# Optimization experiments

Measured on AMD Instinct MI355X. Metric: run time of the kernel, lower is better.

## Reference

```python
import jax, jax.numpy as jnp
import numpy as np

B, T, F, U, OUT_STEPS = 128, 256, 64, 1024, 32
D_HID = 32  # dense head hidden width


def lstm_step(h, c, x, W, R, b):
    # Keras gate order: i, f, g (cell candidate), o
    z = x @ W + h @ R + b  # [B, 4U]
    i, f, g, o = jnp.split(z, 4, axis=-1)
    c_new = jax.nn.sigmoid(f) * c + jax.nn.sigmoid(i) * jnp.tanh(g)
    h_new = jax.nn.sigmoid(o) * jnp.tanh(c_new)
    return h_new, c_new


def setup_inputs() -> dict:
    key = jax.random.key(0)
    ks = jax.random.split(key, 16)
    s = 0.05  # small init scale to keep gates unsaturated
    return {
        "inputs": jax.random.normal(ks[0], (B, T, F), jnp.float32),
        # encoder LSTM layer (input dim F)
        "Wl": jax.random.normal(ks[1], (F, 4 * U), jnp.float32) * s,
        "Rl": jax.random.normal(ks[2], (U, 4 * U), jnp.float32) * s,
        "bl": jnp.zeros((4 * U,), jnp.float32),
        "Wc": jax.random.normal(ks[3], (F, 4 * U), jnp.float32) * s,
        "Rc": jax.random.normal(ks[4], (U, 4 * U), jnp.float32) * s,
        "bc": jnp.zeros((4 * U,), jnp.float32),
        # rnn_cell (an LSTMCell; input dim = units, fed lstm_cell output)
        "Wr": jax.random.normal(ks[5], (U, 4 * U), jnp.float32) * s,
        "Rr": jax.random.normal(ks[6], (U, 4 * U), jnp.float32) * s,
        "br": jnp.zeros((4 * U,), jnp.float32),
        # dense head: Dense(32, relu) -> Dense(num_features)
        "W1": jax.random.normal(ks[7], (U, D_HID), jnp.float32) * s,
        "b1": jnp.zeros((D_HID,), jnp.float32),
        "W2": jax.random.normal(ks[8], (D_HID, F), jnp.float32) * s,
        "b2": jnp.zeros((F,), jnp.float32),
    }


def reference(inputs, Wl, Rl, bl, Wc, Rc, bc, Wr, Rr, br, W1, b1, W2, b2):
    b = inputs.shape[0]
    h0 = jnp.zeros((b, U), inputs.dtype)
    c0 = jnp.zeros((b, U), inputs.dtype)

    def enc_step(carry, x_t):
        h, c = carry
        h, c = lstm_step(h, c, x_t, Wl, Rl, bl)
        return (h, c), None

    # encoder LSTM over time (scan over T, batch-parallel)
    (h, c), _ = jax.lax.scan(enc_step, (h0, c0), jnp.swapaxes(inputs, 0, 1))

    dense = lambda x: jax.nn.relu(x @ W1 + b1) @ W2 + b2

    pred0 = dense(h)  # [B, F]
    # state_rnn initialized from encoder final state (same values, evolves separately)
    init = (pred0, h, c, h, c)

    def ar_step(carry, _):
        pred, hl, cl, hr, cr = carry
        hl, cl = lstm_step(hl, cl, pred, Wc, Rc, bc)
        hr, cr = lstm_step(hr, cr, hl, Wr, Rr, br)
        pred = dense(hr)
        return (pred, hl, cl, hr, cr), pred

    _, preds = jax.lax.scan(ar_step, init, None, length=OUT_STEPS - 1)
    preds = jnp.concatenate([pred0[None], preds], axis=0)  # [OUT, B, F]
    return jnp.transpose(preds, (1, 0, 2))  # [B, OUT, F]
```

## Files before the change

### kernel.cpp

```cpp
#include <hip/hip_runtime.h>

typedef unsigned short u16;
typedef unsigned int u32;
typedef unsigned long long u64;
typedef short v8s __attribute__((ext_vector_type(8)));
typedef int v4i __attribute__((ext_vector_type(4)));
typedef float f32x4 __attribute__((ext_vector_type(4)));

#define NB 128
#define NU 1024
#define NF 64
#define NT 256
#define NOUT 32
#define NBLK 256
#define XS 72
#define FPAD 32
#define ZBS 66

__device__ __forceinline__ u16 f2bf(float f) {
  union { float f; u32 u; } v; v.f = f;
  u32 x = v.u;
  return (u16)((x + 0x7fffu + ((x >> 16) & 1u)) >> 16);
}
__device__ __forceinline__ float bf2f(u16 u) {
  union { u32 u; float f; } v; v.u = ((u32)u) << 16;
  return v.f;
}

__device__ __forceinline__ void cstore32(u32* p, u32 v) {
  __hip_atomic_store(p, v, __ATOMIC_RELAXED, __HIP_MEMORY_SCOPE_AGENT);
}
__device__ __forceinline__ v4i cload128(const void* p) {
  v4i r;
  asm volatile("global_load_dwordx4 %0, %1, off sc0 sc1" : "=v"(r) : "v"(p) : "memory");
  return r;
}

__device__ __forceinline__ void publish(u32* bar, u32 gen, int bid, int tid) {
  asm volatile("s_waitcnt vmcnt(0)" ::: "memory");
  __syncthreads();
  if (tid == 0)
    __hip_atomic_store(&bar[bid * FPAD], gen, __ATOMIC_RELAXED, __HIP_MEMORY_SCOPE_AGENT);
}

__device__ __forceinline__ void pollslice(const u32* bar, u32 gen, int grp,
                                          int w, int lane) {
  const u32* fl = bar + (size_t)(grp * 64 + w * 16 + (lane & 15)) * FPAD;
  bool ok = (lane >= 16);
  u32 spin = 0;
  for (;;) {
    if (!ok)
      ok = __hip_atomic_load(fl, __ATOMIC_RELAXED, __HIP_MEMORY_SCOPE_AGENT) >= gen;
    if (__all(ok)) break;
    __builtin_amdgcn_s_sleep(1);
    if (++spin > 4000000u) break;
  }
}

__global__ void init_bar(u32* bar) {
  int i = blockIdx.x * 256 + threadIdx.x;
  if (i < 2 * NBLK * FPAD) bar[i] = 0;
}

__global__ void pack_weights(const float* __restrict__ top, const float* __restrict__ R,
                             int ktop, int nchunk, u16* __restrict__ dst) {
  int line = blockIdx.x * 256 + threadIdx.x;
  int l = line & 63;
  int rest = line >> 6;
  int s = rest & 1; rest >>= 1;
  int kk = rest % nchunk;
  int t  = rest / nchunk;
  if (t >= 256) return;
  int kbase = kk * 64 + s * 32 + (l >> 4) * 8;
  int col = ((l >> 2) & 3) * 1024 + t * 4 + (l & 3);
  v8s o;
#pragma unroll
  for (int j = 0; j < 8; ++j) {
    int k = kbase + j;
    float v = (k < ktop) ? top[(size_t)k * 4096 + col]
                         : R[(size_t)(k - ktop) * 4096 + col];
    o[j] = (short)f2bf(v);
  }
  *(v8s*)(void*)(dst + (size_t)line * 8) = o;
}

__global__ void pack_w1(const float* __restrict__ W1, u16* __restrict__ dst) {
  int id = blockIdx.x * 256 + threadIdx.x;
  int lane = id & 63;
  int line = id >> 6;
  int res = line >> 6;
  int cl = line & 63;
  int c = cl >> 1, nt = cl & 1;
  int krow = c * 32 + ((lane >> 4) * 8);
  int col = nt * 16 + (lane & 15);
  v8s o;
#pragma unroll
  for (int j = 0; j < 8; ++j) {
    float v = W1[(size_t)(krow + j) * 32 + col];
    u16 hi = f2bf(v);
    o[j] = (short)(res ? f2bf(v - bf2f(hi)) : hi);
  }
  *(v8s*)(void*)(dst + (size_t)id * 8) = o;
}

struct P {
  const float* x;
  const u16 *packE, *packC, *packR, *W1f;
  const float *bl, *bc, *br, *b1, *W2, *b2;
  u16 *hxE0, *hxE1, *hxL0, *hxL1, *hxR0, *hxR1;
  float* out;
  u32* bar;
};

__device__ __forceinline__ v8s ldA(const u16* Asb, int row, int unit) {
  return *(const v8s*)(const void*)(Asb + row * 2048 + ((unit ^ (row & 7)) * 8));
}

__device__ __forceinline__ void stage_bar1(u16* Asb, const u32* bar, u32 gen,
                                           int grp, int w, int lane,
                                           const u16* hx, int dstu) {
  pollslice(bar, gen, grp, w, lane);
  v4i t[16];
#pragma unroll
  for (int j = 0; j < 16; ++j) {
    int q = (w * 16 + j) * 64 + lane;
    t[j] = cload128(hx + (size_t)q * 8);
  }
  asm volatile("s_waitcnt vmcnt(0)" ::: "memory");
#pragma unroll
  for (int j = 0; j < 16; ++j) {
    int q = (w * 16 + j) * 64 + lane;
    int sb = q >> 6, rem = q & 63;
    int r = rem >> 1, c8 = rem & 1;
    int u = (dstu + sb * 2 + c8) ^ (r & 7);
    *(v4i*)(void*)(Asb + r * 2048 + u * 8) = t[j];
  }
  __syncthreads();
}

__device__ __forceinline__ void stage_bar2(u16* Asb, const u32* bar, u32 gen,
                                           int grp, int w, int lane,
                                           const u16* hxa, const u16* hxb) {
  pollslice(bar, gen, grp, w, lane);
  v4i a[16], b[16];
#pragma unroll
  for (int j = 0; j < 16; ++j) {
    int q = (w * 16 + j) * 64 + lane;
    a[j] = cload128(hxa + (size_t)q * 8);
  }
#pragma unroll
  for (int j = 0; j < 16; ++j) {
    int q = (w * 16 + j) * 64 + lane;
    b[j] = cload128(hxb + (size_t)q * 8);
  }
  asm volatile("s_waitcnt vmcnt(0)" ::: "memory");
#pragma unroll
  for (int j = 0; j < 16; ++j) {
    int q = (w * 16 + j) * 64 + lane;
    int sb = q >> 6, rem = q & 63;
    int r = rem >> 1, c8 = rem & 1;
    int u = (sb * 2 + c8) ^ (r & 7);
    *(v4i*)(void*)(Asb + r * 2048 + u * 8) = a[j];
  }
#pragma unroll
  for (int j = 0; j < 16; ++j) {
    int q = (w * 16 + j) * 64 + lane;
    int sb = q >> 6, rem = q & 63;
    int r = rem >> 1, c8 = rem & 1;
    int u = (128 + sb * 2 + c8) ^ (r & 7);
    *(v4i*)(void*)(Asb + r * 2048 + u * 8) = b[j];
  }
  __syncthreads();
}

__device__ __forceinline__ void stageX(u16* Xsb, int tid, int m0,
                                       const float* x, int t) {
#pragma unroll
  for (int i = 0; i < 4; ++i) {
    int idx = tid + i * 256;
    int ml = idx >> 5, dw = idx & 31;
    const float* sp = x + ((size_t)(m0 + ml) * NT + t) * NF + dw * 2;
    u32 v = (u32)f2bf(sp[0]) | ((u32)f2bf(sp[1]) << 16);
    *(u32*)(void*)(Xsb + ml * XS + dw * 2) = v;
  }
}

template <int NCH, int XCH>
__device__ __forceinline__ void mfmaSK(f32x4 (&acc)[4][2], const u16* Asb,
                                       const u16* Xsb, const u16* pack,
                                       int linesz, int tile0,
                                       int w, int lane, int quad, int l15) {
  const u16* tb0 = pack + (size_t)(tile0 + 0) * linesz;
  const u16* tb1 = pack + (size_t)(tile0 + 1) * linesz;
  const u16* tb2 = pack + (size_t)(tile0 + 2) * linesz;
  const u16* tb3 = pack + (size_t)(tile0 + 3) * linesz;
  for (int j = w; j < NCH; j += 4) {
    v8s a0, a1;
    if (XCH > 0 && j < XCH) {
      a0 = *(const v8s*)(const void*)(Xsb + l15 * XS + j * 32 + quad * 8);
      a1 = *(const v8s*)(const void*)(Xsb + (16 + l15) * XS + j * 32 + quad * 8);
    } else {
      int u = (j - XCH) * 4 + quad;
      a0 = ldA(Asb, l15, u);
      a1 = ldA(Asb, 16 + l15, u);
    }
    size_t bo = (size_t)(j * 64 + lane) * 8;
    v8s b0 = *(const v8s*)(const void*)(tb0 + bo);
    v8s b1 = *(const v8s*)(const void*)(tb1 + bo);
    v8s b2 = *(const v8s*)(const void*)(tb2 + bo);
    v8s b3 = *(const v8s*)(const void*)(tb3 + bo);
    acc[0][0] = __builtin_amdgcn_mfma_f32_16x16x32_bf16(a0, b0, acc[0][0], 0, 0, 0);
    acc[1][0] = __builtin_amdgcn_mfma_f32_16x16x32_bf16(a0, b1, acc[1][0], 0, 0, 0);
    acc[2][0] = __builtin_amdgcn_mfma_f32_16x16x32_bf16(a0, b2, acc[2][0], 0, 0, 0);
    acc[3][0] = __builtin_amdgcn_mfma_f32_16x16x32_bf16(a0, b3, acc[3][0], 0, 0, 0);
    acc[0][1] = __builtin_amdgcn_mfma_f32_16x16x32_bf16(a1, b0, acc[0][1], 0, 0, 0);
    acc[1][1] = __builtin_amdgcn_mfma_f32_16x16x32_bf16(a1, b1, acc[1][1], 0, 0, 0);
    acc[2][1] = __builtin_amdgcn_mfma_f32_16x16x32_bf16(a1, b2, acc[2][1], 0, 0, 0);
    acc[3][1] = __builtin_amdgcn_mfma_f32_16x16x32_bf16(a1, b3, acc[3][1], 0, 0, 0);
  }
}

__device__ __forceinline__ void gates_store(float* zb, u16* hpk,
                                            int w, int lane, int quad, int l15,
                                            int wgn, int bid,
                                            const f32x4 (&acc)[4][2],
                                            const float* bias,
                                            float cpair[2], u16* hxout, bool czero) {
  __syncthreads();
#pragma unroll
  for (int tt = 0; tt < 4; ++tt)
#pragma unroll
    for (int rt = 0; rt < 2; ++rt)
#pragma unroll
      for (int r = 0; r < 4; ++r)
        zb[(size_t)(w * 32 + rt * 16 + quad * 4 + r) * ZBS + tt * 16 + l15] =
            acc[tt][rt][r];
  __syncthreads();
  const int tblk = wgn * 4 + w;
#pragma unroll
  for (int rep = 0; rep < 2; ++rep) {
    int pp = lane + rep * 64;
    int ml = pp >> 2;
    int cc = pp & 3;
    int col = tblk * 4 + cc;
    float zg[4];
#pragma unroll
    for (int g = 0; g < 4; ++g) {
      int zc = w * 16 + g * 4 + cc;
      float s = zb[(size_t)(0 * 32 + ml) * ZBS + zc] +
                zb[(size_t)(1 * 32 + ml) * ZBS + zc] +
                zb[(size_t)(2 * 32 + ml) * ZBS + zc] +
                zb[(size_t)(3 * 32 + ml) * ZBS + zc];
      zg[g] = s + bias[g * 1024 + col];
    }
    float cold = czero ? 0.f : cpair[rep];
    float si = 1.f / (1.f + __expf(-zg[0]));
    float sf = 1.f / (1.f + __expf(-zg[1]));
    float so = 1.f / (1.f + __expf(-zg[3]));
    float e2g = __expf(2.f * zg[2]);
    float tg  = (e2g - 1.f) / (e2g + 1.f);
    float cn  = sf * cold + si * tg;
    float e2c = __expf(2.f * cn);
    float tc  = (e2c - 1.f) / (e2c + 1.f);
    cpair[rep] = cn;
    hpk[w * 128 + ml * 4 + cc] = f2bf(so * tc);
  }
  __syncthreads();
  {
    int tid = w * 64 + lane;
    int r = tid >> 3, c2 = tid & 7;
    int wsrc = c2 >> 1;
    u32 v = *(const u32*)(const void*)(hpk + wsrc * 128 + r * 4 + (c2 & 1) * 2);
    cstore32((u32*)(void*)(hxout + (size_t)bid * 512) + r * 8 + c2, v);
  }
}

__device__ __forceinline__ void dense_head(const P& p, const u16* Asb, float* d1s,
                                           u16* Xsb, int tid, int w, int lane,
                                           int quad, int l15, int m0, int step,
                                           bool wout) {
  const int rt = w >> 1, ct = w & 1;
  const int arow = rt * 16 + l15;
  const u16* wf = p.W1f;
  f32x4 acc0 = {0.f, 0.f, 0.f, 0.f}, acc1 = acc0;
#pragma unroll
  for (int k = 0; k < 16; ++k) {
    v8s b0 = *(const v8s*)(const void*)(wf + ((size_t)((2 * k) * 2 + ct) * 64 + lane) * 8);
    v8s a0 = ldA(Asb, arow, 128 + (2 * k) * 4 + quad);
    v8s b1 = *(const v8s*)(const void*)(wf + ((size_t)((2 * k + 1) * 2 + ct) * 64 + lane) * 8);
    v8s a1 = ldA(Asb, arow, 128 + (2 * k + 1) * 4 + quad);
    acc0 = __builtin_amdgcn_mfma_f32_16x16x32_bf16(a0, b0, acc0, 0, 0, 0);
    acc1 = __builtin_amdgcn_mfma_f32_16x16x32_bf16(a1, b1, acc1, 0, 0, 0);
  }
#pragma unroll
  for (int k = 0; k < 16; ++k) {
    v8s b0 = *(const v8s*)(const void*)(wf + ((size_t)(64 + (2 * k) * 2 + ct) * 64 + lane) * 8);
    v8s a0 = ldA(Asb, arow, 128 + (2 * k) * 4 + quad);
    v8s b1 = *(const v8s*)(const void*)(wf + ((size_t)(64 + (2 * k + 1) * 2 + ct) * 64 + lane) * 8);
    v8s a1 = ldA(Asb, arow, 128 + (2 * k + 1) * 4 + quad);
    acc0 = __builtin_amdgcn_mfma_f32_16x16x32_bf16(a0, b0, acc0, 0, 0, 0);
    acc1 = __builtin_amdgcn_mfma_f32_16x16x32_bf16(a1, b1, acc1, 0, 0, 0);
  }
  acc0 += acc1;
  const int col = ct * 16 + l15;
  const float b1c = p.b1[col];
#pragma unroll
  for (int r = 0; r < 4; ++r) {
    int row = rt * 16 + quad * 4 + r;
    d1s[row * 33 + col] = fmaxf(acc0[r] + b1c, 0.f);
  }
  __syncthreads();
  const int r = tid >> 3, cb = (tid & 7) * 8;
  float s2[8];
#pragma unroll
  for (int cc = 0; cc < 8; ++cc) s2[cc] = p.b2[cb + cc];
#pragma unroll
  for (int k = 0; k < 32; ++k) {
    float dv = d1s[r * 33 + k];
    f32x4 w20 = *(const f32x4*)(const void*)(p.W2 + k * 64 + cb);
    f32x4 w21 = *(const f32x4*)(const void*)(p.W2 + k * 64 + cb + 4);
    s2[0] += dv * w20[0]; s2[1] += dv * w20[1];
    s2[2] += dv * w20[2]; s2[3] += dv * w20[3];
    s2[4] += dv * w21[0]; s2[5] += dv * w21[1];
    s2[6] += dv * w21[2]; s2[7] += dv * w21[3];
  }
#pragma unroll
  for (int cc = 0; cc < 8; ++cc) Xsb[r * XS + cb + cc] = f2bf(s2[cc]);
  if (wout) {
    float* po = p.out + ((size_t)(m0 + r) * NOUT + step) * NF + cb;
#pragma unroll
    for (int cc = 0; cc < 8; ++cc) po[cc] = s2[cc];
  }
  __syncthreads();
}

__global__ void __launch_bounds__(256, 1) rnn_persist(P p) {
  __shared__ __align__(16) u16 Asb[32 * 2048];
  __shared__ __align__(16) u16 Xsb[32 * XS];
  __shared__ float d1s[32 * 33];
  __shared__ u16 hpack[512];
  float* zb = (float*)(void*)Asb;

  const int tid = threadIdx.x;
  const int bid = blockIdx.x;
  const int wgn = bid & 63;
  const int mg  = bid >> 6;
  const int m0  = mg * 32;
  const int w    = tid >> 6;
  const int lane = tid & 63;
  const int quad = lane >> 4;
  const int l15  = lane & 15;
  const int tile0 = wgn * 4;
  const size_t gsl = (size_t)mg * 64 * 512;

  float cE2[2] = {0.f, 0.f};
  u32 bno = 0;

  stageX(Xsb, tid, m0, p.x, 0);
  for (int t = 0; t < NT; ++t) {
    const u16* hread = ((t & 1) ? p.hxE1 : p.hxE0) + gsl;
    u16* hwrite      = (t & 1) ? p.hxE0 : p.hxE1;
    f32x4 acc[4][2];
#pragma unroll
    for (int a = 0; a < 4; ++a)
#pragma unroll
      for (int b = 0; b < 2; ++b) acc[a][b] = (f32x4){0.f, 0.f, 0.f, 0.f};
    if (t > 0) {
      stage_bar1(Asb, p.bar, bno, mg, w, lane, hread, 0);
      mfmaSK<34, 2>(acc, Asb, Xsb, p.packE, 17408, tile0, w, lane, quad, l15);
    } else {
      __syncthreads();
      mfmaSK<2, 2>(acc, Asb, Xsb, p.packE, 17408, tile0, w, lane, quad, l15);
    }
    gates_store(zb, hpack, w, lane, quad, l15, wgn, bid, acc,
                p.bl, cE2, hwrite, t == 0);
    if (t + 1 < NT) stageX(Xsb, tid, m0, p.x, t + 1);
    publish(p.bar, ++bno, bid, tid);
  }

  float cL2[2] = {cE2[0], cE2[1]};
  float cR2[2] = {cE2[0], cE2[1]};
  for (int s = 1; s < NOUT; ++s) {
    const u16* hlr = ((s == 1) ? p.hxE0 : ((s & 1) ? p.hxL1 : p.hxL0)) + gsl;
    const u16* hrd = ((s == 1) ? p.hxE0 : ((s & 1) ? p.hxR1 : p.hxR0)) + gsl;
    u16* hlw = (s & 1) ? p.hxL0 : p.hxL1;
    u16* hrw = (s & 1) ? p.hxR0 : p.hxR1;

    {
      stage_bar2(Asb, p.bar, bno, mg, w, lane, hlr, hrd);
      dense_head(p, Asb, d1s, Xsb, tid, w, lane, quad, l15, m0, s - 1, wgn == 0);
      f32x4 acc[4][2];
#pragma unroll
      for (int a = 0; a < 4; ++a)
#pragma unroll
        for (int b = 0; b < 2; ++b) acc[a][b] = (f32x4){0.f, 0.f, 0.f, 0.f};
      mfmaSK<34, 2>(acc, Asb, Xsb, p.packC, 17408, tile0, w, lane, quad, l15);
      gates_store(zb, hpack, w, lane, quad, l15, wgn, bid, acc,
                  p.bc, cL2, hlw, false);
    }
    publish(p.bar, ++bno, bid, tid);

    {
      stage_bar2(Asb, p.bar, bno, mg, w, lane, hlw + gsl, hrd);
      f32x4 acc[4][2];
#pragma unroll
      for (int a = 0; a < 4; ++a)
#pragma unroll
        for (int b = 0; b < 2; ++b) acc[a][b] = (f32x4){0.f, 0.f, 0.f, 0.f};
      mfmaSK<64, 0>(acc, Asb, Xsb, p.packR, 32768, tile0, w, lane, quad, l15);
      gates_store(zb, hpack, w, lane, quad, l15, wgn, bid, acc,
                  p.br, cR2, hrw, false);
    }
    publish(p.bar, ++bno, bid, tid);
  }

  if (wgn == 0) {
    stage_bar1(Asb, p.bar, bno, mg, w, lane, p.hxR0 + gsl, 128);
    dense_head(p, Asb, d1s, Xsb, tid, w, lane, quad, l15, m0, NOUT - 1, true);
  }
}

extern "C" void kernel_launch(void* const* d_in, const int* in_sizes, int n_in,
                              void* d_out, int out_size, void* d_ws, size_t ws_size,
                              hipStream_t stream) {
  const float* x  = (const float*)d_in[0];
  const float* Wl = (const float*)d_in[1];
  const float* Rl = (const float*)d_in[2];
  const float* bl = (const float*)d_in[3];
  const float* Wc = (const float*)d_in[4];
  const float* Rc = (const float*)d_in[5];
  const float* bc = (const float*)d_in[6];
  const float* Wr = (const float*)d_in[7];
  const float* Rr = (const float*)d_in[8];
  const float* br = (const float*)d_in[9];
  const float* W1 = (const float*)d_in[10];
  const float* b1 = (const float*)d_in[11];
  const float* W2 = (const float*)d_in[12];
  const float* b2 = (const float*)d_in[13];

  char* ws = (char*)d_ws;
  size_t off = 0;
  auto alloc = [&](size_t bytes) -> void* {
    void* r = ws + off;
    off += (bytes + 255) & ~(size_t)255;
    return r;
  };
  const size_t szPackE = (size_t)256 * 17408 * 2;
  const size_t szPackR = (size_t)256 * 32768 * 2;
  const size_t szHx    = (size_t)NBLK * 512 * 2;
  u16* packE = (u16*)alloc(szPackE);
  u16* packC = (u16*)alloc(szPackE);
  u16* packR = (u16*)alloc(szPackR);
  u16* W1f   = (u16*)alloc((size_t)128 * 64 * 8 * 2);
  u16* hxE0 = (u16*)alloc(szHx);
  u16* hxE1 = (u16*)alloc(szHx);
  u16* hxL0 = (u16*)alloc(szHx);
  u16* hxL1 = (u16*)alloc(szHx);
  u16* hxR0 = (u16*)alloc(szHx);
  u16* hxR1 = (u16*)alloc(szHx);
  u32* bar = (u32*)alloc(2 * NBLK * FPAD * 4);

  init_bar<<<dim3(64), dim3(256), 0, stream>>>(bar);
  pack_weights<<<dim3(128 * 17), dim3(256), 0, stream>>>(Wl, Rl, 64, 17, packE);
  pack_weights<<<dim3(128 * 17), dim3(256), 0, stream>>>(Wc, Rc, 64, 17, packC);
  pack_weights<<<dim3(128 * 32), dim3(256), 0, stream>>>(Wr, Rr, 1024, 32, packR);
  pack_w1<<<dim3(32), dim3(256), 0, stream>>>(W1, W1f);

  static P p;
  p.x = x;
  p.packE = packE; p.packC = packC; p.packR = packR; p.W1f = W1f;
  p.bl = bl; p.bc = bc; p.br = br;
  p.b1 = b1; p.W2 = W2; p.b2 = b2;
  p.hxE0 = hxE0; p.hxE1 = hxE1;
  p.hxL0 = hxL0; p.hxL1 = hxL1;
  p.hxR0 = hxR0; p.hxR1 = hxR1;
  p.out = (float*)d_out;
  p.bar = bar;

  rnn_persist<<<dim3(NBLK), dim3(256), 0, stream>>>(p);
}
```

Measured before the change: 3.014 ms.

## Split batch across twice as many persistent blocks, 16 rows each

Doubles the persistent grid to 512 blocks, so each block handles 16 batch rows instead of 32. The staging, MFMA accumulators, gate epilogue and dense head are reworked for the smaller tile, and launch bounds now allow two blocks per CU. This aims to spread the serial recurrent work across more CUs and shrink each block's per-step latency. In exchange, every block streams the same weight tiles from L2, so weight traffic doubles, and more blocks must meet at each grid barrier, which adds synchronisation cost.

```diff
diff --git a/kernel.cpp b/kernel.cpp
--- a/kernel.cpp
+++ b/kernel.cpp
@@ -12,7 +12,7 @@
 #define NF 64
 #define NT 256
 #define NOUT 32
-#define NBLK 256
+#define NBLK 512
 #define XS 72
 #define FPAD 32
 #define ZBS 66
@@ -59,7 +59,7 @@
 
 __global__ void init_bar(u32* bar) {
   int i = blockIdx.x * 256 + threadIdx.x;
-  if (i < 2 * NBLK * FPAD) bar[i] = 0;
+  if (i < NBLK * FPAD) bar[i] = 0;
 }
 
 __global__ void pack_weights(const float* __restrict__ top, const float* __restrict__ R,
@@ -120,19 +120,20 @@
                                            int grp, int w, int lane,
                                            const u16* hx, int dstu) {
   pollslice(bar, gen, grp, w, lane);
-  v4i t[16];
-#pragma unroll
-  for (int j = 0; j < 16; ++j) {
-    int q = (w * 16 + j) * 64 + lane;
-    t[j] = cload128(hx + (size_t)q * 8);
+  v4i t[8];
+#pragma unroll
+  for (int j = 0; j < 8; ++j) {
+    int ul = j * 64 + lane;
+    int pl = ul >> 5, q = ul & 31;
+    t[j] = cload128(hx + (size_t)((w * 16 + pl) * 32 + q) * 8);
   }
   asm volatile("s_waitcnt vmcnt(0)" ::: "memory");
 #pragma unroll
-  for (int j = 0; j < 16; ++j) {
-    int q = (w * 16 + j) * 64 + lane;
-    int sb = q >> 6, rem = q & 63;
-    int r = rem >> 1, c8 = rem & 1;
-    int u = (dstu + sb * 2 + c8) ^ (r & 7);
+  for (int j = 0; j < 8; ++j) {
+    int ul = j * 64 + lane;
+    int pl = ul >> 5, q = ul & 31;
+    int r = q >> 1, c8 = q & 1;
+    int u = (dstu + (w * 16 + pl) * 2 + c8) ^ (r & 7);
     *(v4i*)(void*)(Asb + r * 2048 + u * 8) = t[j];
   }
   __syncthreads();
@@ -142,32 +143,34 @@
                                            int grp, int w, int lane,
                                            const u16* hxa, const u16* hxb) {
   pollslice(bar, gen, grp, w, lane);
-  v4i a[16], b[16];
-#pragma unroll
-  for (int j = 0; j < 16; ++j) {
-    int q = (w * 16 + j) * 64 + lane;
-    a[j] = cload128(hxa + (size_t)q * 8);
-  }
-#pragma unroll
-  for (int j = 0; j < 16; ++j) {
-    int q = (w * 16 + j) * 64 + lane;
-    b[j] = cload128(hxb + (size_t)q * 8);
+  v4i a[8], b[8];
+#pragma unroll
+  for (int j = 0; j < 8; ++j) {
+    int ul = j * 64 + lane;
+    int pl = ul >> 5, q = ul & 31;
+    a[j] = cload128(hxa + (size_t)((w * 16 + pl) * 32 + q) * 8);
+  }
+#pragma unroll
+  for (int j = 0; j < 8; ++j) {
+    int ul = j * 64 + lane;
+    int pl = ul >> 5, q = ul & 31;
+    b[j] = cload128(hxb + (size_t)((w * 16 + pl) * 32 + q) * 8);
   }
   asm volatile("s_waitcnt vmcnt(0)" ::: "memory");
 #pragma unroll
-  for (int j = 0; j < 16; ++j) {
-    int q = (w * 16 + j) * 64 + lane;
-    int sb = q >> 6, rem = q & 63;
-    int r = rem >> 1, c8 = rem & 1;
-    int u = (sb * 2 + c8) ^ (r & 7);
+  for (int j = 0; j < 8; ++j) {
+    int ul = j * 64 + lane;
+    int pl = ul >> 5, q = ul & 31;
+    int r = q >> 1, c8 = q & 1;
+    int u = ((w * 16 + pl) * 2 + c8) ^ (r & 7);
     *(v4i*)(void*)(Asb + r * 2048 + u * 8) = a[j];
   }
 #pragma unroll
-  for (int j = 0; j < 16; ++j) {
-    int q = (w * 16 + j) * 64 + lane;
-    int sb = q >> 6, rem = q & 63;
-    int r = rem >> 1, c8 = rem & 1;
-    int u = (128 + sb * 2 + c8) ^ (r & 7);
+  for (int j = 0; j < 8; ++j) {
+    int ul = j * 64 + lane;
+    int pl = ul >> 5, q = ul & 31;
+    int r = q >> 1, c8 = q & 1;
+    int u = (128 + (w * 16 + pl) * 2 + c8) ^ (r & 7);
     *(v4i*)(void*)(Asb + r * 2048 + u * 8) = b[j];
   }
   __syncthreads();
@@ -176,7 +179,7 @@
 __device__ __forceinline__ void stageX(u16* Xsb, int tid, int m0,
                                        const float* x, int t) {
 #pragma unroll
-  for (int i = 0; i < 4; ++i) {
+  for (int i = 0; i < 2; ++i) {
     int idx = tid + i * 256;
     int ml = idx >> 5, dw = idx & 31;
     const float* sp = x + ((size_t)(m0 + ml) * NT + t) * NF + dw * 2;
@@ -186,7 +189,7 @@
 }
 
 template <int NCH, int XCH>
-__device__ __forceinline__ void mfmaSK(f32x4 (&acc)[4][2], const u16* Asb,
+__device__ __forceinline__ void mfmaSK(f32x4 (&acc)[4], const u16* Asb,
                                        const u16* Xsb, const u16* pack,
                                        int linesz, int tile0,
                                        int w, int lane, int quad, int l15) {
@@ -195,65 +198,52 @@
   const u16* tb2 = pack + (size_t)(tile0 + 2) * linesz;
   const u16* tb3 = pack + (size_t)(tile0 + 3) * linesz;
   for (int j = w; j < NCH; j += 4) {
-    v8s a0, a1;
+    v8s a0;
     if (XCH > 0 && j < XCH) {
       a0 = *(const v8s*)(const void*)(Xsb + l15 * XS + j * 32 + quad * 8);
-      a1 = *(const v8s*)(const void*)(Xsb + (16 + l15) * XS + j * 32 + quad * 8);
     } else {
-      int u = (j - XCH) * 4 + quad;
-      a0 = ldA(Asb, l15, u);
-      a1 = ldA(Asb, 16 + l15, u);
+      a0 = ldA(Asb, l15, (j - XCH) * 4 + quad);
     }
     size_t bo = (size_t)(j * 64 + lane) * 8;
     v8s b0 = *(const v8s*)(const void*)(tb0 + bo);
     v8s b1 = *(const v8s*)(const void*)(tb1 + bo);
     v8s b2 = *(const v8s*)(const void*)(tb2 + bo);
     v8s b3 = *(const v8s*)(const void*)(tb3 + bo);
-    acc[0][0] = __builtin_amdgcn_mfma_f32_16x16x32_bf16(a0, b0, acc[0][0], 0, 0, 0);
-    acc[1][0] = __builtin_amdgcn_mfma_f32_16x16x32_bf16(a0, b1, acc[1][0], 0, 0, 0);
-    acc[2][0] = __builtin_amdgcn_mfma_f32_16x16x32_bf16(a0, b2, acc[2][0], 0, 0, 0);
-    acc[3][0] = __builtin_amdgcn_mfma_f32_16x16x32_bf16(a0, b3, acc[3][0], 0, 0, 0);
-    acc[0][1] = __builtin_amdgcn_mfma_f32_16x16x32_bf16(a1, b0, acc[0][1], 0, 0, 0);
-    acc[1][1] = __builtin_amdgcn_mfma_f32_16x16x32_bf16(a1, b1, acc[1][1], 0, 0, 0);
-    acc[2][1] = __builtin_amdgcn_mfma_f32_16x16x32_bf16(a1, b2, acc[2][1], 0, 0, 0);
-    acc[3][1] = __builtin_amdgcn_mfma_f32_16x16x32_bf16(a1, b3, acc[3][1], 0, 0, 0);
+    acc[0] = __builtin_amdgcn_mfma_f32_16x16x32_bf16(a0, b0, acc[0], 0, 0, 0);
+    acc[1] = __builtin_amdgcn_mfma_f32_16x16x32_bf16(a0, b1, acc[1], 0, 0, 0);
+    acc[2] = __builtin_amdgcn_mfma_f32_16x16x32_bf16(a0, b2, acc[2], 0, 0, 0);
+    acc[3] = __builtin_amdgcn_mfma_f32_16x16x32_bf16(a0, b3, acc[3], 0, 0, 0);
   }
 }
 
 __device__ __forceinline__ void gates_store(float* zb, u16* hpk,
                                             int w, int lane, int quad, int l15,
-                                            int wgn, int bid,
-                                            const f32x4 (&acc)[4][2],
+                                            int wgn, int bid, int tid,
+                                            const f32x4 (&acc)[4],
                                             const float* bias,
-                                            float cpair[2], u16* hxout, bool czero) {
+                                            float& creg, u16* hxout, bool czero) {
   __syncthreads();
 #pragma unroll
   for (int tt = 0; tt < 4; ++tt)
 #pragma unroll
-    for (int rt = 0; rt < 2; ++rt)
-#pragma unroll
-      for (int r = 0; r < 4; ++r)
-        zb[(size_t)(w * 32 + rt * 16 + quad * 4 + r) * ZBS + tt * 16 + l15] =
-            acc[tt][rt][r];
-  __syncthreads();
-  const int tblk = wgn * 4 + w;
-#pragma unroll
-  for (int rep = 0; rep < 2; ++rep) {
-    int pp = lane + rep * 64;
-    int ml = pp >> 2;
-    int cc = pp & 3;
-    int col = tblk * 4 + cc;
+    for (int r = 0; r < 4; ++r)
+      zb[(size_t)(w * 16 + quad * 4 + r) * ZBS + tt * 16 + l15] = acc[tt][r];
+  __syncthreads();
+  {
+    int r = tid >> 4, hc = tid & 15;
+    int tt = hc >> 2, cc = hc & 3;
+    int col = wgn * 16 + hc;
     float zg[4];
 #pragma unroll
     for (int g = 0; g < 4; ++g) {
-      int zc = w * 16 + g * 4 + cc;
-      float s = zb[(size_t)(0 * 32 + ml) * ZBS + zc] +
-                zb[(size_t)(1 * 32 + ml) * ZBS + zc] +
-                zb[(size_t)(2 * 32 + ml) * ZBS + zc] +
-                zb[(size_t)(3 * 32 + ml) * ZBS + zc];
+      int zc = tt * 16 + g * 4 + cc;
+      float s = zb[(size_t)(0 * 16 + r) * ZBS + zc] +
+                zb[(size_t)(1 * 16 + r) * ZBS + zc] +
+                zb[(size_t)(2 * 16 + r) * ZBS + zc] +
+                zb[(size_t)(3 * 16 + r) * ZBS + zc];
       zg[g] = s + bias[g * 1024 + col];
     }
-    float cold = czero ? 0.f : cpair[rep];
+    float cold = czero ? 0.f : creg;
     float si = 1.f / (1.f + __expf(-zg[0]));
     float sf = 1.f / (1.f + __expf(-zg[1]));
     float so = 1.f / (1.f + __expf(-zg[3]));
@@ -262,16 +252,14 @@
     float cn  = sf * cold + si * tg;
     float e2c = __expf(2.f * cn);
     float tc  = (e2c - 1.f) / (e2c + 1.f);
-    cpair[rep] = cn;
-    hpk[w * 128 + ml * 4 + cc] = f2bf(so * tc);
-  }
-  __syncthreads();
-  {
-    int tid = w * 64 + lane;
-    int r = tid >> 3, c2 = tid & 7;
-    int wsrc = c2 >> 1;
-    u32 v = *(const u32*)(const void*)(hpk + wsrc * 128 + r * 4 + (c2 & 1) * 2);
-    cstore32((u32*)(void*)(hxout + (size_t)bid * 512) + r * 8 + c2, v);
+    creg = cn;
+    hpk[r * 16 + hc] = f2bf(so * tc);
+  }
+  __syncthreads();
+  if (tid < 128) {
+    int rr = tid >> 3, c2 = tid & 7;
+    u32 v = *(const u32*)(const void*)(hpk + rr * 16 + c2 * 2);
+    cstore32((u32*)(void*)(hxout + (size_t)bid * 256) + rr * 8 + c2, v);
   }
 }
 
@@ -279,107 +267,90 @@
                                            u16* Xsb, int tid, int w, int lane,
                                            int quad, int l15, int m0, int step,
                                            bool wout) {
-  const int rt = w >> 1, ct = w & 1;
-  const int arow = rt * 16 + l15;
+  const int nt = w & 1, kp = w >> 1;
   const u16* wf = p.W1f;
-  f32x4 acc0 = {0.f, 0.f, 0.f, 0.f}, acc1 = acc0;
+  f32x4 aH = {0.f, 0.f, 0.f, 0.f}, aL = aH;
 #pragma unroll
   for (int k = 0; k < 16; ++k) {
-    v8s b0 = *(const v8s*)(const void*)(wf + ((size_t)((2 * k) * 2 + ct) * 64 + lane) * 8);
-    v8s a0 = ldA(Asb, arow, 128 + (2 * k) * 4 + quad);
-    v8s b1 = *(const v8s*)(const void*)(wf + ((size_t)((2 * k + 1) * 2 + ct) * 64 + lane) * 8);
-    v8s a1 = ldA(Asb, arow, 128 + (2 * k + 1) * 4 + quad);
-    acc0 = __builtin_amdgcn_mfma_f32_16x16x32_bf16(a0, b0, acc0, 0, 0, 0);
-    acc1 = __builtin_amdgcn_mfma_f32_16x16x32_bf16(a1, b1, acc1, 0, 0, 0);
-  }
-#pragma unroll
-  for (int k = 0; k < 16; ++k) {
-    v8s b0 = *(const v8s*)(const void*)(wf + ((size_t)(64 + (2 * k) * 2 + ct) * 64 + lane) * 8);
-    v8s a0 = ldA(Asb, arow, 128 + (2 * k) * 4 + quad);
-    v8s b1 = *(const v8s*)(const void*)(wf + ((size_t)(64 + (2 * k + 1) * 2 + ct) * 64 + lane) * 8);
-    v8s a1 = ldA(Asb, arow, 128 + (2 * k + 1) * 4 + quad);
-    acc0 = __builtin_amdgcn_mfma_f32_16x16x32_bf16(a0, b0, acc0, 0, 0, 0);
-    acc1 = __builtin_amdgcn_mfma_f32_16x16x32_bf16(a1, b1, acc1, 0, 0, 0);
-  }
-  acc0 += acc1;
-  const int col = ct * 16 + l15;
-  const float b1c = p.b1[col];
-#pragma unroll
-  for (int r = 0; r < 4; ++r) {
-    int row = rt * 16 + quad * 4 + r;
-    d1s[row * 33 + col] = fmaxf(acc0[r] + b1c, 0.f);
-  }
-  __syncthreads();
-  const int r = tid >> 3, cb = (tid & 7) * 8;
-  float s2[8];
-#pragma unroll
-  for (int cc = 0; cc < 8; ++cc) s2[cc] = p.b2[cb + cc];
-#pragma unroll
-  for (int k = 0; k < 32; ++k) {
-    float dv = d1s[r * 33 + k];
-    f32x4 w20 = *(const f32x4*)(const void*)(p.W2 + k * 64 + cb);
-    f32x4 w21 = *(const f32x4*)(const void*)(p.W2 + k * 64 + cb + 4);
-    s2[0] += dv * w20[0]; s2[1] += dv * w20[1];
-    s2[2] += dv * w20[2]; s2[3] += dv * w20[3];
-    s2[4] += dv * w21[0]; s2[5] += dv * w21[1];
-    s2[6] += dv * w21[2]; s2[7] += dv * w21[3];
-  }
-#pragma unroll
-  for (int cc = 0; cc < 8; ++cc) Xsb[r * XS + cb + cc] = f2bf(s2[cc]);
-  if (wout) {
-    float* po = p.out + ((size_t)(m0 + r) * NOUT + step) * NF + cb;
-#pragma unroll
-    for (int cc = 0; cc < 8; ++cc) po[cc] = s2[cc];
-  }
-  __syncthreads();
-}
-
-__global__ void __launch_bounds__(256, 1) rnn_persist(P p) {
-  __shared__ __align__(16) u16 Asb[32 * 2048];
-  __shared__ __align__(16) u16 Xsb[32 * XS];
-  __shared__ float d1s[32 * 33];
-  __shared__ u16 hpack[512];
+    int c = kp + 2 * k;
+    v8s a  = ldA(Asb, l15, 128 + c * 4 + quad);
+    v8s bh = *(const v8s*)(const void*)(wf + ((size_t)(c * 2 + nt) * 64 + lane) * 8);
+    v8s bl = *(const v8s*)(const void*)(wf + ((size_t)(64 + c * 2 + nt) * 64 + lane) * 8);
+    aH = __builtin_amdgcn_mfma_f32_16x16x32_bf16(a, bh, aH, 0, 0, 0);
+    aL = __builtin_amdgcn_mfma_f32_16x16x32_bf16(a, bl, aL, 0, 0, 0);
+  }
+  aH += aL;
+#pragma unroll
+  for (int r = 0; r < 4; ++r)
+    d1s[kp * 528 + (quad * 4 + r) * 33 + nt * 16 + l15] = aH[r];
+  __syncthreads();
+  {
+    int r = tid >> 4, cb = (tid & 15) * 4;
+    float s2[4];
+#pragma unroll
+    for (int j = 0; j < 4; ++j) s2[j] = p.b2[cb + j];
+#pragma unroll
+    for (int k = 0; k < 32; ++k) {
+      float dv = fmaxf(d1s[r * 33 + k] + d1s[528 + r * 33 + k] + p.b1[k], 0.f);
+      f32x4 w2 = *(const f32x4*)(const void*)(p.W2 + k * 64 + cb);
+      s2[0] += dv * w2[0]; s2[1] += dv * w2[1];
+      s2[2] += dv * w2[2]; s2[3] += dv * w2[3];
+    }
+#pragma unroll
+    for (int j = 0; j < 4; ++j) Xsb[r * XS + cb + j] = f2bf(s2[j]);
+    if (wout) {
+      float* po = p.out + ((size_t)(m0 + r) * NOUT + step) * NF + cb;
+#pragma unroll
+      for (int j = 0; j < 4; ++j) po[j] = s2[j];
+    }
+  }
+  __syncthreads();
+}
+
+__global__ void __launch_bounds__(256, 2) rnn_persist(P p) {
+  __shared__ __align__(16) u16 Asb[16 * 2048];
+  __shared__ __align__(16) u16 Xsb[16 * XS];
+  __shared__ float d1s[2 * 16 * 33];
+  __shared__ u16 hpack[256];
   float* zb = (float*)(void*)Asb;
 
   const int tid = threadIdx.x;
   const int bid = blockIdx.x;
   const int wgn = bid & 63;
-  const int mg  = bid >> 6;
-  const int m0  = mg * 32;
+  const int grp = bid >> 6;
+  const int m0  = grp * 16;
   const int w    = tid >> 6;
   const int lane = tid & 63;
   const int quad = lane >> 4;
   const int l15  = lane & 15;
   const int tile0 = wgn * 4;
-  const size_t gsl = (size_t)mg * 64 * 512;
-
-  float cE2[2] = {0.f, 0.f};
+  const size_t gsl = (size_t)grp * 64 * 256;
+
+  float cE = 0.f;
   u32 bno = 0;
 
   stageX(Xsb, tid, m0, p.x, 0);
   for (int t = 0; t < NT; ++t) {
     const u16* hread = ((t & 1) ? p.hxE1 : p.hxE0) + gsl;
     u16* hwrite      = (t & 1) ? p.hxE0 : p.hxE1;
-    f32x4 acc[4][2];
-#pragma unroll
-    for (int a = 0; a < 4; ++a)
-#pragma unroll
-      for (int b = 0; b < 2; ++b) acc[a][b] = (f32x4){0.f, 0.f, 0.f, 0.f};
+    f32x4 acc[4];
+#pragma unroll
+    for (int a = 0; a < 4; ++a) acc[a] = (f32x4){0.f, 0.f, 0.f, 0.f};
     if (t > 0) {
-      stage_bar1(Asb, p.bar, bno, mg, w, lane, hread, 0);
+      stage_bar1(Asb, p.bar, bno, grp, w, lane, hread, 0);
       mfmaSK<34, 2>(acc, Asb, Xsb, p.packE, 17408, tile0, w, lane, quad, l15);
     } else {
       __syncthreads();
       mfmaSK<2, 2>(acc, Asb, Xsb, p.packE, 17408, tile0, w, lane, quad, l15);
     }
-    gates_store(zb, hpack, w, lane, quad, l15, wgn, bid, acc,
-                p.bl, cE2, hwrite, t == 0);
+    gates_store(zb, hpack, w, lane, quad, l15, wgn, bid, tid, acc,
+                p.bl, cE, hwrite, t == 0);
     if (t + 1 < NT) stageX(Xsb, tid, m0, p.x, t + 1);
     publish(p.bar, ++bno, bid, tid);
   }
 
-  float cL2[2] = {cE2[0], cE2[1]};
-  float cR2[2] = {cE2[0], cE2[1]};
+  float cL = cE;
+  float cR = cE;
   for (int s = 1; s < NOUT; ++s) {
     const u16* hlr = ((s == 1) ? p.hxE0 : ((s & 1) ? p.hxL1 : p.hxL0)) + gsl;
     const u16* hrd = ((s == 1) ? p.hxE0 : ((s & 1) ? p.hxR1 : p.hxR0)) + gsl;
@@ -387,35 +358,31 @@
     u16* hrw = (s & 1) ? p.hxR0 : p.hxR1;
 
     {
-      stage_bar2(Asb, p.bar, bno, mg, w, lane, hlr, hrd);
+      stage_bar2(Asb, p.bar, bno, grp, w, lane, hlr, hrd);
       dense_head(p, Asb, d1s, Xsb, tid, w, lane, quad, l15, m0, s - 1, wgn == 0);
-      f32x4 acc[4][2];
-#pragma unroll
-      for (int a = 0; a < 4; ++a)
-#pragma unroll
-        for (int b = 0; b < 2; ++b) acc[a][b] = (f32x4){0.f, 0.f, 0.f, 0.f};
+      f32x4 acc[4];
+#pragma unroll
+      for (int a = 0; a < 4; ++a) acc[a] = (f32x4){0.f, 0.f, 0.f, 0.f};
       mfmaSK<34, 2>(acc, Asb, Xsb, p.packC, 17408, tile0, w, lane, quad, l15);
-      gates_store(zb, hpack, w, lane, quad, l15, wgn, bid, acc,
-                  p.bc, cL2, hlw, false);
+      gates_store(zb, hpack, w, lane, quad, l15, wgn, bid, tid, acc,
+                  p.bc, cL, hlw, false);
     }
     publish(p.bar, ++bno, bid, tid);
 
     {
-      stage_bar2(Asb, p.bar, bno, mg, w, lane, hlw + gsl, hrd);
-      f32x4 acc[4][2];
-#pragma unroll
-      for (int a = 0; a < 4; ++a)
-#pragma unroll
-        for (int b = 0; b < 2; ++b) acc[a][b] = (f32x4){0.f, 0.f, 0.f, 0.f};
+      stage_bar2(Asb, p.bar, bno, grp, w, lane, hlw + gsl, hrd);
+      f32x4 acc[4];
+#pragma unroll
+      for (int a = 0; a < 4; ++a) acc[a] = (f32x4){0.f, 0.f, 0.f, 0.f};
       mfmaSK<64, 0>(acc, Asb, Xsb, p.packR, 32768, tile0, w, lane, quad, l15);
-      gates_store(zb, hpack, w, lane, quad, l15, wgn, bid, acc,
-                  p.br, cR2, hrw, false);
+      gates_store(zb, hpack, w, lane, quad, l15, wgn, bid, tid, acc,
+                  p.br, cR, hrw, false);
     }
     publish(p.bar, ++bno, bid, tid);
   }
 
   if (wgn == 0) {
-    stage_bar1(Asb, p.bar, bno, mg, w, lane, p.hxR0 + gsl, 128);
+    stage_bar1(Asb, p.bar, bno, grp, w, lane, p.hxR0 + gsl, 128);
     dense_head(p, Asb, d1s, Xsb, tid, w, lane, quad, l15, m0, NOUT - 1, true);
   }
 }
@@ -447,7 +414,7 @@
   };
   const size_t szPackE = (size_t)256 * 17408 * 2;
   const size_t szPackR = (size_t)256 * 32768 * 2;
-  const size_t szHx    = (size_t)NBLK * 512 * 2;
+  const size_t szHx    = (size_t)NBLK * 256 * 2;
   u16* packE = (u16*)alloc(szPackE);
   u16* packC = (u16*)alloc(szPackE);
   u16* packR = (u16*)alloc(szPackR);
@@ -458,7 +425,7 @@
   u16* hxL1 = (u16*)alloc(szHx);
   u16* hxR0 = (u16*)alloc(szHx);
   u16* hxR1 = (u16*)alloc(szHx);
-  u32* bar = (u32*)alloc(2 * NBLK * FPAD * 4);
+  u32* bar = (u32*)alloc((size_t)NBLK * FPAD * 4);
 
   init_bar<<<dim3(64), dim3(256), 0, stream>>>(bar);
   pack_weights<<<dim3(128 * 17), dim3(256), 0, stream>>>(Wl, Rl, 64, 17, packE);
```

Measured after the change: 2.711 ms. 1.11x faster.
